# Performance work log

Hardware: AMD Instinct MI355X
Metric: run time of the kernel (lower is better)

## Reference

```python
import jax, jax.numpy as jnp
import numpy as np

M = 4        # num_modalities
C = 128      # in_channels
NH = 4       # num_heads
HD = C // NH # head_dim = 32
OUT = 128    # out_channels
B, D, H, W = 1, 12, 12, 12
N = D * H * W
EPS = 1e-5
SCALE = float(np.sqrt(HD))


def setup_inputs() -> dict:
    key = jax.random.key(0)
    ks = jax.random.split(key, 12)
    inp = {}
    for i in range(M):
        inp[f"feat{i}"] = jax.random.normal(ks[i], (B, C, D, H, W), dtype=jnp.float32)
    s = 1.0 / np.sqrt(C)
    inp["Wq"] = jax.random.normal(ks[4], (M, C, C), dtype=jnp.float32) * s
    inp["Wk"] = jax.random.normal(ks[5], (M, C, C), dtype=jnp.float32) * s
    inp["Wv"] = jax.random.normal(ks[6], (M, C, C), dtype=jnp.float32) * s
    inp["Wout"] = jax.random.normal(ks[7], (OUT, C), dtype=jnp.float32) * s
    inp["bn_gamma"] = jnp.ones((OUT,), jnp.float32)
    inp["bn_beta"] = jnp.zeros((OUT,), jnp.float32)
    inp["bn_mean"] = jax.random.normal(ks[8], (OUT,), dtype=jnp.float32) * 0.1
    inp["bn_var"] = jax.random.uniform(ks[9], (OUT,), dtype=jnp.float32, minval=0.5, maxval=1.5)
    return inp


def _proj(Wm, feats):
    # per-modality 1x1 conv == matmul over channels: [M,C,C] x [M,B,C,N] -> [M,B,nh,N,hd]
    p = jnp.einsum('moc,mbcn->mbon', Wm, feats)
    return p.reshape(M, B, NH, HD, N).transpose(0, 1, 2, 4, 3)


def reference(feat0, feat1, feat2, feat3, Wq, Wk, Wv, Wout,
              bn_gamma, bn_beta, bn_mean, bn_var):
    feats = jnp.stack([feat0, feat1, feat2, feat3]).reshape(M, B, C, N)
    Q = _proj(Wq, feats)   # [M,B,nh,N,hd]
    K = _proj(Wk, feats)
    V = _proj(Wv, feats)
    # concat K/V over modalities along token axis -> [B,nh,M*N,hd]
    Kall = K.transpose(1, 2, 0, 3, 4).reshape(B, NH, M * N, HD)
    Vall = V.transpose(1, 2, 0, 3, 4).reshape(B, NH, M * N, HD)
    fused = jnp.zeros((B, NH, N, HD), jnp.float32)
    for i in range(M):  # small fixed loop over modalities
        attn = jnp.einsum('bhqd,bhkd->bhqk', Q[i], Kall) / SCALE  # [B,nh,N,M*N]
        attn = jax.nn.softmax(attn, axis=-1)  # dropout is identity at eval
        fused = fused + jnp.einsum('bhqk,bhkd->bhqd', attn, Vall)
    fused = fused.transpose(0, 1, 3, 2).reshape(B, C, N)
    # out_proj: 1x1 Conv3d -> BN (eval, running stats) -> ReLU
    y = jnp.einsum('oc,bcn->bon', Wout, fused)
    inv = bn_gamma / jnp.sqrt(bn_var + EPS)
    y = y * inv[None, :, None] + (bn_beta - bn_mean * inv)[None, :, None]
    return jax.nn.relu(y).reshape(B, OUT, D, H, W)
```

## Files before the change

kernel.cpp:

```cpp
#include <hip/hip_runtime.h>

#define MODS 4
#define CH   128
#define NHD  4
#define HDIM 32
#define NTOK 1728
#define NKEY (MODS*NTOK)
#define NT   27
#define QSC (0.17677669529663687f * 1.4426950408889634f)

#ifndef __has_builtin
#define __has_builtin(x) 0
#endif
#if __has_builtin(__builtin_amdgcn_exp2f)
#define EXP2(x) __builtin_amdgcn_exp2f(x)
#else
#define EXP2(x) __expf(0.69314718055994531f * (x))
#endif

typedef __bf16 bf16x8 __attribute__((ext_vector_type(8)));
typedef float  f32x16 __attribute__((ext_vector_type(16)));
typedef unsigned int u32x4 __attribute__((ext_vector_type(4)));

__device__ inline bf16x8 ldb8(const unsigned short* p) {
    return *reinterpret_cast<const bf16x8*>(p);
}
__device__ inline unsigned short bfc(float x) {
    return __builtin_bit_cast(unsigned short, (__bf16)x);
}
__device__ inline unsigned int pkbf(float a, float b) {
    return (unsigned int)bfc(a) | ((unsigned int)bfc(b) << 16);
}
__device__ inline bf16x8 cvt8(const float* p, float sc) {
    float4 x = *reinterpret_cast<const float4*>(p);
    float4 y = *reinterpret_cast<const float4*>(p + 4);
    u32x4 u = {pkbf(x.x * sc, x.y * sc), pkbf(x.z * sc, x.w * sc),
               pkbf(y.x * sc, y.y * sc), pkbf(y.z * sc, y.w * sc)};
    return __builtin_bit_cast(bf16x8, u);
}
__device__ inline void glds16(const unsigned short* g, unsigned short* l) {
    __builtin_amdgcn_global_load_lds(
        (const __attribute__((address_space(1))) unsigned int*)(g),
        (__attribute__((address_space(3))) unsigned int*)(l), 16, 0, 0);
}

__global__ __launch_bounds__(256) void proj_kernel(
    const float* __restrict__ f0, const float* __restrict__ f1,
    const float* __restrict__ f2, const float* __restrict__ f3,
    const float* __restrict__ Wq, const float* __restrict__ Wk,
    const float* __restrict__ Wv,
    unsigned short* __restrict__ Qb, unsigned short* __restrict__ Kb,
    unsigned short* __restrict__ V2)
{
    __shared__ __align__(16) unsigned short fT[32][136];
    __shared__ __align__(16) float accf[128 * 33];

    const int tid = threadIdx.x;
    const int lane = tid & 63;
    const int w    = tid >> 6;
    const int l31  = lane & 31;
    const int hi   = lane >> 5;

    const int bid = blockIdx.x;
    const int tm  = bid / 54;
    const int nb  = (bid % 54) * 32;
    const int t   = tm >> 2, m = tm & 3;

    const float* fsrc = (m == 0) ? f0 : (m == 1) ? f1 : (m == 2) ? f2 : f3;
    const float* Wsrc = ((t == 0) ? Wq : (t == 1) ? Wk : Wv) + (size_t)m * CH * CH;
    const float  wsc  = (t == 0) ? QSC : 1.0f;

    {
        const int n = tid & 31, cg = tid >> 5;
        float v[16];
        #pragma unroll
        for (int k = 0; k < 16; ++k)
            v[k] = fsrc[(size_t)(cg * 16 + k) * NTOK + nb + n];
        unsigned int* dst = reinterpret_cast<unsigned int*>(&fT[n][cg * 16]);
        #pragma unroll
        for (int j = 0; j < 8; ++j) dst[j] = pkbf(v[2 * j], v[2 * j + 1]);
    }
    __syncthreads();

    const float* Wrow = Wsrc + (size_t)(w * 32 + l31) * CH + hi * 8;
    f32x16 acc;
    #pragma unroll
    for (int r = 0; r < 16; ++r) acc[r] = 0.f;
    #pragma unroll
    for (int cc = 0; cc < 8; ++cc) {
        bf16x8 a = cvt8(Wrow + cc * 16, wsc);
        bf16x8 b = ldb8(&fT[l31][cc * 16 + hi * 8]);
        acc = __builtin_amdgcn_mfma_f32_32x32x16_bf16(a, b, acc, 0, 0, 0);
    }
    #pragma unroll
    for (int r = 0; r < 16; ++r) {
        const int orow = w * 32 + (r & 3) + 8 * (r >> 2) + 4 * hi;
        accf[orow * 33 + l31] = acc[r];
    }
    __syncthreads();

    if (t < 2) {
        unsigned short* dstb = (t == 0) ? Qb : Kb;
        const int nl = tid >> 3, dp = (tid & 7) * 4;
        #pragma unroll
        for (int h = 0; h < 4; ++h) {
            ushort4 pk;
            pk.x = bfc(accf[(h * 32 + dp + 0) * 33 + nl]);
            pk.y = bfc(accf[(h * 32 + dp + 1) * 33 + nl]);
            pk.z = bfc(accf[(h * 32 + dp + 2) * 33 + nl]);
            pk.w = bfc(accf[(h * 32 + dp + 3) * 33 + nl]);
            *reinterpret_cast<ushort4*>(
                dstb + (((size_t)(m * NHD + h)) * NTOK + nb + nl) * HDIM + dp) = pk;
        }
    } else {
        const int row = tid >> 1, half = tid & 1;
        const int nw = half * 16;
        unsigned short* dst = V2 + (size_t)row * NKEY + (size_t)m * NTOK + nb + nw;
        const float* src = &accf[row * 33 + nw];
        ushort4 p0, p1, p2, p3;
        p0.x = bfc(src[0]);  p0.y = bfc(src[1]);  p0.z = bfc(src[2]);  p0.w = bfc(src[3]);
        p1.x = bfc(src[8]);  p1.y = bfc(src[9]);  p1.z = bfc(src[10]); p1.w = bfc(src[11]);
        p2.x = bfc(src[4]);  p2.y = bfc(src[5]);  p2.z = bfc(src[6]);  p2.w = bfc(src[7]);
        p3.x = bfc(src[12]); p3.y = bfc(src[13]); p3.z = bfc(src[14]); p3.w = bfc(src[15]);
        *reinterpret_cast<ushort4*>(dst + 0)  = p0;
        *reinterpret_cast<ushort4*>(dst + 4)  = p1;
        *reinterpret_cast<ushort4*>(dst + 8)  = p2;
        *reinterpret_cast<ushort4*>(dst + 12) = p3;
    }
}

__global__ __launch_bounds__(256, 6) void attn_kernel(
    const unsigned short* __restrict__ Qb, const unsigned short* __restrict__ Kb,
    const unsigned short* __restrict__ V2,
    float* __restrict__ accT, float* __restrict__ sR)
{
    __shared__ __align__(16) unsigned short smAll[2][2][2][1024];

    const int tid  = threadIdx.x;
    const int lane = tid & 63;
    const int w    = tid >> 6;
    const int qslot = w & 1;
    const int ks    = w >> 1;
    const int l31  = lane & 31;
    const int hi   = lane >> 5;

    const int bid  = blockIdx.x;
    const int slot = bid & 7;
    const int h    = slot >> 1;
    const int ko   = slot & 1;
    const int rest = bid >> 3;
    const int qb   = rest % 108;
    const int kseg = rest / 108;
    const int qtile = qb * 2 + qslot;
    const int qg0  = qtile * 32;
    const int im   = qg0 / NTOK;
    const int n0   = qg0 % NTOK;
    const int km   = ko * 2 + ks;
    const int p    = kseg * 2 + ko;

    const unsigned short* qp = Qb + (((size_t)(im * NHD + h)) * NTOK + n0 + l31) * HDIM + hi * 8;
    const bf16x8 qf0 = ldb8(qp);
    const bf16x8 qf1 = ldb8(qp + 16);

    const int rk0 = qslot * 16 + (lane >> 2);
    const int ck0 = (lane & 3) ^ ((rk0 >> 1) & 3);
    const unsigned short* gk0 = Kb
        + (((size_t)(km * NHD + h)) * NTOK + kseg * 864 + rk0) * HDIM + ck0 * 8;
    const int dv0 = qslot * 16 + (lane >> 2);
    const int cv0 = (lane & 3) ^ (dv0 & 3);
    const unsigned short* gv0 = V2
        + ((size_t)(h * HDIM + dv0)) * NKEY + km * NTOK + kseg * 864 + cv0 * 8;

    const int fK = (l31 >> 1) & 3, fV = l31 & 3;
    const int kA0 = l31 * 32 + ((hi ^ fK) << 3);
    const int kB0 = l31 * 32 + (((2 + hi) ^ fK) << 3);
    const int vo0 = l31 * 32 + ((hi ^ fV) << 3);
    const int vo1 = l31 * 32 + (((2 + hi) ^ fV) << 3);

    f32x16 z;
    #pragma unroll
    for (int r = 0; r < 16; ++r) z[r] = 0.f;
    f32x16 o_acc = z, s_acc = z;
    bf16x8 onesv;
    #pragma unroll
    for (int j = 0; j < 8; ++j) onesv[j] = (__bf16)1.0f;

    #define STAGE(bb) do {                                      \
        glds16(gk0, &smAll[bb][ks][0][0] + qslot * 512);        \
        glds16(gv0, &smAll[bb][ks][1][0] + qslot * 512);        \
        gk0 += 1024; gv0 += 32;                                 \
    } while (0)

    STAGE(0);
    __syncthreads();

    int buf = 0;
    for (int t = 0; t < NT; ++t) {
        if (t + 1 < NT) STAGE(buf ^ 1);
        const unsigned short* Kl = &smAll[buf][ks][0][0];
        const unsigned short* Vl = &smAll[buf][ks][1][0];

        bf16x8 k0 = ldb8(Kl + kA0);
        bf16x8 k1 = ldb8(Kl + kB0);
        f32x16 c = __builtin_amdgcn_mfma_f32_32x32x16_bf16(k0, qf0, z, 0, 0, 0);
        c = __builtin_amdgcn_mfma_f32_32x32x16_bf16(k1, qf1, c, 0, 0, 0);

        float e[16];
        #pragma unroll
        for (int r = 0; r < 16; ++r) e[r] = EXP2(c[r]);
        bf16x8 pa0, pa1;
        #pragma unroll
        for (int j = 0; j < 8; ++j) { pa0[j] = (__bf16)e[j]; pa1[j] = (__bf16)e[8 + j]; }

        bf16x8 v0 = ldb8(Vl + vo0);
        bf16x8 v1 = ldb8(Vl + vo1);

        o_acc = __builtin_amdgcn_mfma_f32_32x32x16_bf16(pa0, v0, o_acc, 0, 0, 0);
        o_acc = __builtin_amdgcn_mfma_f32_32x32x16_bf16(pa1, v1, o_acc, 0, 0, 0);
        s_acc = __builtin_amdgcn_mfma_f32_32x32x16_bf16(pa0, onesv, s_acc, 0, 0, 0);
        s_acc = __builtin_amdgcn_mfma_f32_32x32x16_bf16(pa1, onesv, s_acc, 0, 0, 0);

        __syncthreads();
        buf ^= 1;
    }
    #undef STAGE

    float* accfL = (float*)&smAll[0][0][0][0];
    if (ks == 1) {
        #pragma unroll
        for (int r = 0; r < 16; ++r) {
            const int qrow = (r & 3) + 8 * (r >> 2) + 4 * hi;
            accfL[(qslot * 32 + qrow) * 33 + l31] = o_acc[r];
            if (l31 == 0) accfL[(qslot * 32 + qrow) * 33 + 32] = s_acc[r];
        }
    }
    __syncthreads();
    if (ks == 0) {
        #pragma unroll
        for (int r = 0; r < 16; ++r) {
            const int qrow = (r & 3) + 8 * (r >> 2) + 4 * hi;
            accfL[(qslot * 32 + qrow) * 33 + l31] += o_acc[r];
            if (l31 == 0) accfL[(qslot * 32 + qrow) * 33 + 32] += s_acc[r];
        }
    }
    __syncthreads();
    {
        const int q  = tid & 63;
        const int dq = tid >> 6;
        #pragma unroll
        for (int j = 0; j < 8; ++j) {
            const int d = dq * 8 + j;
            accT[((size_t)((p * 4 + h) * HDIM + d)) * NKEY + (size_t)qb * 64 + q]
                = accfL[q * 33 + d];
        }
        if (tid < 64)
            sR[((size_t)(p * 4 + h)) * NKEY + (size_t)qb * 64 + tid] = accfL[tid * 33 + 32];
    }
}

__global__ __launch_bounds__(512) void normout_kernel(
    const float* __restrict__ accT, const float* __restrict__ sR,
    const float* __restrict__ Wout,
    const float* __restrict__ gamma, const float* __restrict__ beta,
    const float* __restrict__ mean,  const float* __restrict__ var,
    float* __restrict__ out)
{
    __shared__ __align__(16) unsigned short fT2[32][136];
    __shared__ float rsL[4][4][32];

    const int tid = threadIdx.x;
    const int nb  = blockIdx.x * 32;

    {
        const int h = tid >> 7, imq = (tid >> 5) & 3, n = tid & 31;
        float s = 0.f;
        #pragma unroll
        for (int pp = 0; pp < 4; ++pp)
            s += sR[(size_t)(pp * 4 + h) * NKEY + (size_t)imq * NTOK + nb + n];
        rsL[h][imq][n] = 1.0f / s;
    }
    __syncthreads();

    {
        const int n4 = (tid & 7) * 4;
        const int c0 = (tid >> 3) * 2;
        const int h  = c0 >> 5;
        float acc4[2][4] = {};
        #pragma unroll
        for (int imq = 0; imq < 4; ++imq) {
            const size_t q = (size_t)imq * NTOK + nb + n4;
            float a[2][4] = {};
            #pragma unroll
            for (int pp = 0; pp < 4; ++pp) {
                #pragma unroll
                for (int cc = 0; cc < 2; ++cc) {
                    const int d = (c0 + cc) & 31;
                    float4 x = *reinterpret_cast<const float4*>(
                        accT + ((size_t)((pp * 4 + h) * HDIM + d)) * NKEY + q);
                    a[cc][0] += x.x; a[cc][1] += x.y; a[cc][2] += x.z; a[cc][3] += x.w;
                }
            }
            #pragma unroll
            for (int cc = 0; cc < 2; ++cc)
                #pragma unroll
                for (int nn = 0; nn < 4; ++nn)
                    acc4[cc][nn] = fmaf(a[cc][nn], rsL[h][imq][n4 + nn], acc4[cc][nn]);
        }
        #pragma unroll
        for (int nn = 0; nn < 4; ++nn) {
            ushort2 pk;
            pk.x = bfc(acc4[0][nn]); pk.y = bfc(acc4[1][nn]);
            *reinterpret_cast<ushort2*>(&fT2[n4 + nn][c0]) = pk;
        }
    }
    __syncthreads();

    if (tid < 256) {
        const int lane = tid & 63;
        const int w    = tid >> 6;
        const int l31  = lane & 31;
        const int hi   = lane >> 5;
        const float* Arow = Wout + (size_t)(w * 32 + l31) * CH + hi * 8;
        f32x16 acc;
        #pragma unroll
        for (int r = 0; r < 16; ++r) acc[r] = 0.f;
        #pragma unroll
        for (int cc = 0; cc < 8; ++cc) {
            bf16x8 a = cvt8(Arow + cc * 16, 1.0f);
            bf16x8 b = ldb8(&fT2[l31][cc * 16 + hi * 8]);
            acc = __builtin_amdgcn_mfma_f32_32x32x16_bf16(a, b, acc, 0, 0, 0);
        }
        #pragma unroll
        for (int r = 0; r < 16; ++r) {
            const int orow = w * 32 + (r & 3) + 8 * (r >> 2) + 4 * hi;
            const float inv = gamma[orow] * rsqrtf(var[orow] + 1e-5f);
            const float sh  = fmaf(-mean[orow], inv, beta[orow]);
            out[(size_t)orow * NTOK + nb + l31] = fmaxf(fmaf(acc[r], inv, sh), 0.f);
        }
    }
}

extern "C" void kernel_launch(void* const* d_in, const int* in_sizes, int n_in,
                              void* d_out, int out_size, void* d_ws, size_t ws_size,
                              hipStream_t stream)
{
    const float* f0    = (const float*)d_in[0];
    const float* f1    = (const float*)d_in[1];
    const float* f2    = (const float*)d_in[2];
    const float* f3    = (const float*)d_in[3];
    const float* Wq    = (const float*)d_in[4];
    const float* Wk    = (const float*)d_in[5];
    const float* Wv    = (const float*)d_in[6];
    const float* Wout  = (const float*)d_in[7];
    const float* gamma = (const float*)d_in[8];
    const float* beta  = (const float*)d_in[9];
    const float* mean  = (const float*)d_in[10];
    const float* var   = (const float*)d_in[11];
    float* out = (float*)d_out;

    const size_t QKV = (size_t)MODS * NHD * NTOK * HDIM;
    unsigned short* Qb  = (unsigned short*)d_ws;
    unsigned short* Kb  = Qb + QKV;
    unsigned short* V2  = Kb + QKV;
    float* accT = (float*)(V2 + QKV);
    float* sR   = accT + (size_t)512 * NKEY;

    proj_kernel<<<648, 256, 0, stream>>>(f0, f1, f2, f3, Wq, Wk, Wv, Qb, Kb, V2);
    attn_kernel<<<1728, 256, 0, stream>>>(Qb, Kb, V2, accT, sR);
    normout_kernel<<<54, 512, 0, stream>>>(
        accT, sR, Wout, gamma, beta, mean, var, out);
}
```

Measured before the change: 65.89 us.

## Give each wave private K/V staging buffers and drop per-iteration block barriers

Each of the four waves now stages its own full 32-key K and V tiles into a private LDS region instead of sharing tiles between the two query-slot waves. Inside the loop, explicit vmcnt/lgkmcnt waits replace the block-wide __syncthreads, so waves run independently. The next-next tile is issued right after the current tile's LDS reads, giving a deeper prefetch. The cost is doubled LDS per block and duplicated global loads across qslot waves, and the occupancy hint drops from 6 to 5 blocks.

After: 71.21 us. +8.1%, slower.

```diff
diff --git a/kernel.cpp b/kernel.cpp
--- a/kernel.cpp
+++ b/kernel.cpp
@@ -129,12 +129,12 @@
     }
 }
 
-__global__ __launch_bounds__(256, 6) void attn_kernel(
+__global__ __launch_bounds__(256, 5) void attn_kernel(
     const unsigned short* __restrict__ Qb, const unsigned short* __restrict__ Kb,
     const unsigned short* __restrict__ V2,
     float* __restrict__ accT, float* __restrict__ sR)
 {
-    __shared__ __align__(16) unsigned short smAll[2][2][2][1024];
+    __shared__ __align__(16) unsigned short smAll[2][4][2][1024];
 
     const int tid  = threadIdx.x;
     const int lane = tid & 63;
@@ -162,14 +162,16 @@
     const bf16x8 qf0 = ldb8(qp);
     const bf16x8 qf1 = ldb8(qp + 16);
 
-    const int rk0 = qslot * 16 + (lane >> 2);
-    const int ck0 = (lane & 3) ^ ((rk0 >> 1) & 3);
-    const unsigned short* gk0 = Kb
-        + (((size_t)(km * NHD + h)) * NTOK + kseg * 864 + rk0) * HDIM + ck0 * 8;
-    const int dv0 = qslot * 16 + (lane >> 2);
-    const int cv0 = (lane & 3) ^ (dv0 & 3);
-    const unsigned short* gv0 = V2
-        + ((size_t)(h * HDIM + dv0)) * NKEY + km * NTOK + kseg * 864 + cv0 * 8;
+    const int rkh = lane >> 2;
+    const int ckk = (lane & 3) ^ ((rkh >> 1) & 3);
+    const unsigned short* gkA = Kb
+        + (((size_t)(km * NHD + h)) * NTOK + kseg * 864 + rkh) * HDIM + ckk * 8;
+    const unsigned short* gkB = gkA + 16 * HDIM;
+    const int dvh = lane >> 2;
+    const int cvv = (lane & 3) ^ (dvh & 3);
+    const unsigned short* gvA = V2
+        + ((size_t)(h * HDIM + dvh)) * NKEY + km * NTOK + kseg * 864 + cvv * 8;
+    const unsigned short* gvB = gvA + (size_t)16 * NKEY;
 
     const int fK = (l31 >> 1) & 3, fV = l31 & 3;
     const int kA0 = l31 * 32 + ((hi ^ fK) << 3);
@@ -186,22 +188,30 @@
     for (int j = 0; j < 8; ++j) onesv[j] = (__bf16)1.0f;
 
     #define STAGE(bb) do {                                      \
-        glds16(gk0, &smAll[bb][ks][0][0] + qslot * 512);        \
-        glds16(gv0, &smAll[bb][ks][1][0] + qslot * 512);        \
-        gk0 += 1024; gv0 += 32;                                 \
+        unsigned short* _k = &smAll[bb][w][0][0];               \
+        glds16(gkA, _k);        glds16(gkB, _k + 512);          \
+        unsigned short* _v = &smAll[bb][w][1][0];               \
+        glds16(gvA, _v);        glds16(gvB, _v + 512);          \
+        gkA += 1024; gkB += 1024; gvA += 32; gvB += 32;         \
     } while (0)
 
     STAGE(0);
-    __syncthreads();
+    STAGE(1);
 
     int buf = 0;
     for (int t = 0; t < NT; ++t) {
-        if (t + 1 < NT) STAGE(buf ^ 1);
-        const unsigned short* Kl = &smAll[buf][ks][0][0];
-        const unsigned short* Vl = &smAll[buf][ks][1][0];
-
+        if (t < NT - 1) asm volatile("s_waitcnt vmcnt(4)" ::: "memory");
+        else            asm volatile("s_waitcnt vmcnt(0)" ::: "memory");
+
+        const unsigned short* Kl = &smAll[buf][w][0][0];
+        const unsigned short* Vl = &smAll[buf][w][1][0];
         bf16x8 k0 = ldb8(Kl + kA0);
         bf16x8 k1 = ldb8(Kl + kB0);
+        bf16x8 v0 = ldb8(Vl + vo0);
+        bf16x8 v1 = ldb8(Vl + vo1);
+        asm volatile("s_waitcnt lgkmcnt(0)" ::: "memory");
+        if (t + 2 < NT) STAGE(buf);
+
         f32x16 c = __builtin_amdgcn_mfma_f32_32x32x16_bf16(k0, qf0, z, 0, 0, 0);
         c = __builtin_amdgcn_mfma_f32_32x32x16_bf16(k1, qf1, c, 0, 0, 0);
 
@@ -211,19 +221,17 @@
         bf16x8 pa0, pa1;
         #pragma unroll
         for (int j = 0; j < 8; ++j) { pa0[j] = (__bf16)e[j]; pa1[j] = (__bf16)e[8 + j]; }
-
-        bf16x8 v0 = ldb8(Vl + vo0);
-        bf16x8 v1 = ldb8(Vl + vo1);
 
         o_acc = __builtin_amdgcn_mfma_f32_32x32x16_bf16(pa0, v0, o_acc, 0, 0, 0);
         o_acc = __builtin_amdgcn_mfma_f32_32x32x16_bf16(pa1, v1, o_acc, 0, 0, 0);
         s_acc = __builtin_amdgcn_mfma_f32_32x32x16_bf16(pa0, onesv, s_acc, 0, 0, 0);
         s_acc = __builtin_amdgcn_mfma_f32_32x32x16_bf16(pa1, onesv, s_acc, 0, 0, 0);
 
-        __syncthreads();
         buf ^= 1;
     }
     #undef STAGE
+
+    __syncthreads();
 
     float* accfL = (float*)&smAll[0][0][0][0];
     if (ks == 1) {
```
